# Performance work log

Hardware: AMD Instinct MI355X
Metric: run time of the kernel (lower is better)

The kernel has to match this reference:

```python
import jax, jax.numpy as jnp
import numpy as np

N = 100000      # nodes
E = 1600000     # directed edges
F_IN = 128      # node feature dim
H = 128         # hidden dim
C = 16          # classes


def setup_inputs() -> dict:
    key = jax.random.key(0)
    ks = jax.random.split(key, 8)
    s = 1.0 / np.sqrt(H)
    return {
        "x": jax.random.normal(ks[0], (N, F_IN), dtype=jnp.float32),
        "edge_index": jax.random.randint(ks[1], (2, E), 0, N, dtype=jnp.int32),
        "W1": jax.random.normal(ks[2], (F_IN, H), dtype=jnp.float32) * s,
        "b1": jnp.zeros((H,), jnp.float32),
        "W2": jax.random.normal(ks[3], (H, H), dtype=jnp.float32) * s,
        "b2": jnp.zeros((H,), jnp.float32),
        "W3": jax.random.normal(ks[4], (H, H), dtype=jnp.float32) * s,
        "b3": jnp.zeros((H,), jnp.float32),
        "Wfc": jax.random.normal(ks[5], (H, C), dtype=jnp.float32) * s,
        "bfc": jnp.zeros((C,), jnp.float32),
    }


def _gcn_conv(x, W, b, src, dst, norm):
    # x' = b + scatter_add over edges of norm * (x @ W)[src] into dst
    h = x @ W                                   # [N, H] dense GEMM
    msg = h[src] * norm[:, None]                # [E+N, H] gather + scale
    out = jax.ops.segment_sum(msg, dst, num_segments=N)  # scatter-add
    return out + b


def reference(x, edge_index, W1, b1, W2, b2, W3, b3, Wfc, bfc):
    loops = jnp.arange(N, dtype=edge_index.dtype)
    src = jnp.concatenate([edge_index[0], loops])   # [E+N] with self-loops
    dst = jnp.concatenate([edge_index[1], loops])
    # symmetric normalization deg^{-1/2}[src] * deg^{-1/2}[dst] (PyG default)
    deg = jax.ops.segment_sum(jnp.ones_like(dst, dtype=x.dtype), dst, num_segments=N)
    dinv = jax.lax.rsqrt(deg)                       # deg >= 1 due to self-loops
    norm = dinv[src] * dinv[dst]

    h = jax.nn.elu(_gcn_conv(x, W1, b1, src, dst, norm))   # dropout is identity in eval
    h = jax.nn.elu(_gcn_conv(h, W2, b2, src, dst, norm))
    h = jax.nn.elu(_gcn_conv(h, W3, b3, src, dst, norm))
    logits = h @ Wfc + bfc                                  # [N, C]
    return jax.nn.log_softmax(logits, axis=-1)
```

## Files before the change

kernel.cpp:

```cpp
#include <hip/hip_runtime.h>
#include <math.h>

#define HDIM 128
#define CDIM 16
#define CAP 48
#define ASTR 136
#define HSTR 132
#define NBINS 256
#define TILE 4096
#define NPBMAX 512
#define SORTCAP 7424

typedef unsigned short u16;
typedef unsigned int u32;
typedef __attribute__((ext_vector_type(8))) short short8;
typedef __attribute__((ext_vector_type(4))) float f32x4;
typedef __attribute__((ext_vector_type(2))) float f32x2;

__device__ inline u16 f2bf(float f) {
  u32 u = __float_as_uint(f);
  u += 0x7fffu + ((u >> 16) & 1u);
  return (u16)(u >> 16);
}
__device__ inline float bf_lo(u32 p) { return __uint_as_float(p << 16); }
__device__ inline float bf_hi(u32 p) { return __uint_as_float(p & 0xffff0000u); }
__device__ inline u32 pack2(float a, float b) {
  return (u32)f2bf(a) | ((u32)f2bf(b) << 16);
}
__device__ inline u32 cvtpk(float a, float b) {
  u32 r;
  asm("v_cvt_pk_bf16_f32 %0, %1, %2" : "=v"(r) : "v"(a), "v"(b));
  return r;
}
__device__ inline void acc_word(f32x2& acc, u32 w) {
  f32x2 x;
  x.x = __uint_as_float(w << 16);
  x.y = __uint_as_float(w & 0xffff0000u);
  asm("v_pk_add_f32 %0, %1, %2" : "=v"(acc) : "v"(x), "v"(acc));
}


__global__ __launch_bounds__(256) void bin_kernel(const int* __restrict__ ei,
                                                  int* __restrict__ cursor,
                                                  u32* __restrict__ bins,
                                                  int binCap, int E, int npb, int nbE,
                                                  int nbW, int N,
                                                  const float* __restrict__ W0,
                                                  const float* __restrict__ W1,
                                                  const float* __restrict__ W2,
                                                  u16* __restrict__ Wt,
                                                  u16* __restrict__ Arow,
                                                  u16* __restrict__ Brow) {
  int tid = threadIdx.x;
  if (blockIdx.x >= nbE) {
    if (blockIdx.x >= nbE + nbW) {
      if (tid < 16) ((uint4*)Arow)[tid] = make_uint4(0, 0, 0, 0);
      else if (tid < 32) ((uint4*)Brow)[tid - 16] = make_uint4(0, 0, 0, 0);
      return;
    }
    int t = (blockIdx.x - nbE) * 256 + tid;
    int which = t >> 14, idx = t & 16383;
    int n = idx >> 7, k = idx & 127;
    const float* W = which == 0 ? W0 : (which == 1 ? W1 : W2);
    Wt[(size_t)which * HDIM * HDIM + n * HDIM + k] = f2bf(W[k * HDIM + n]);
    return;
  }
  __shared__ u32 eds32[TILE];
  __shared__ u32 srt[TILE];
  __shared__ unsigned char bid[TILE];
  __shared__ int hist[NBINS], lbase[NBINS + 1], gbase[NBINS], rnk[NBINS];
  int t0 = blockIdx.x * TILE;
  int n = min(TILE, E - t0);
  hist[tid] = 0;
  rnk[tid] = 0;
  __syncthreads();
  for (int i = tid; i < n; i += 256) {
    int s = ei[t0 + i];
    int d = ei[E + t0 + i];
    int b = d / npb;
    eds32[i] = ((u32)(d - b * npb) << 17) | (u32)s;
    bid[i] = (unsigned char)b;
    atomicAdd(&hist[b], 1);
  }
  __syncthreads();
  int h = hist[tid];
  lbase[tid] = h;
  __syncthreads();
#pragma unroll
  for (int off = 1; off < 256; off <<= 1) {
    int v = tid >= off ? lbase[tid - off] : 0;
    __syncthreads();
    lbase[tid] += v;
    __syncthreads();
  }
  int ex = lbase[tid] - h;
  __syncthreads();
  lbase[tid] = ex;
  if (tid == 255) lbase[256] = ex + h;
  gbase[tid] = h ? atomicAdd(&cursor[tid], h) : 0;
  __syncthreads();
  for (int i = tid; i < n; i += 256) {
    int b = bid[i];
    int r = lbase[b] + atomicAdd(&rnk[b], 1);
    srt[r] = eds32[i];
  }
  __syncthreads();
  for (int i = tid; i < n; i += 256) {
    int lo = 0, hi = 255;
#pragma unroll
    for (int k = 0; k < 8; ++k) {
      int mid = (lo + hi + 1) >> 1;
      if (lbase[mid] <= i) lo = mid; else hi = mid - 1;
    }
    int r = gbase[lo] + (i - lbase[lo]);
    if (r < binCap) bins[(size_t)lo * binCap + r] = srt[i];
  }
}

__global__ __launch_bounds__(256) void fill2_kernel(const u32* __restrict__ bins,
                                                    const int* __restrict__ cursor,
                                                    int binCap, int npb,
                                                    int* __restrict__ deg,
                                                    int* __restrict__ csr, int N) {
  __shared__ int hist[NPBMAX];
  __shared__ int base[NPBMAX + 1];
  __shared__ int sorted[SORTCAP];
  int b = blockIdx.x;
  int tid = threadIdx.x;
  int n0 = b * npb;
  int nn = min(npb, N - n0);
  if (nn <= 0) return;
  int cnt = min(min(cursor[b], binCap), SORTCAP);
  const u32* eb = bins + (size_t)b * binCap;
  for (int i = tid; i < nn; i += 256) hist[i] = 0;
  __syncthreads();
  for (int i = tid; i < cnt; i += 256) atomicAdd(&hist[eb[i] >> 17], 1);
  __syncthreads();
  if (tid == 0) {
    int s = 0;
    for (int i = 0; i < nn; ++i) { base[i] = s; s += hist[i]; }
    base[nn] = s;
  }
  __syncthreads();
  for (int i = tid; i < nn; i += 256) hist[i] = 0;
  __syncthreads();
  for (int i = tid; i < cnt; i += 256) {
    u32 w = eb[i];
    int loc = w >> 17;
    sorted[base[loc] + atomicAdd(&hist[loc], 1)] = (int)(w & 0x1FFFFu);
  }
  __syncthreads();
  for (int i = tid; i < nn; i += 256) deg[n0 + i] = base[i + 1] - base[i];
  int total = nn * CAP;
  int* cout = csr + (size_t)n0 * CAP;
  for (int i = tid; i < total; i += 256) {
    int loc = (int)(((u32)(i >> 4) * 21846u) >> 16);
    int j = i - loc * CAP;
    int s0 = base[loc];
    int dc = min(base[loc + 1] - s0, CAP);
    cout[i] = j < dc ? sorted[s0 + j] : N;
  }
}


template <bool FP32IN>
__global__ __launch_bounds__(256) void gemm_k(const void* __restrict__ Xv,
                                              const u16* __restrict__ Wt,
                                              const int* __restrict__ deg,
                                              u16* __restrict__ G, int N) {
  __shared__ u16 As[64 * ASTR];
  __shared__ u16 Wsm[128 * ASTR];
  int tid = threadIdx.x;
  int row0 = blockIdx.x * 64;

  {
    int r = tid >> 2, c = tid & 3;
    int rg = row0 + r;
    if (rg >= N) rg = N - 1;
    uint4* dst = (uint4*)(As + r * ASTR + c * 32);
    if (FP32IN) {
      const float4* src = (const float4*)((const float*)Xv + (size_t)rg * HDIM + c * 32);
#pragma unroll
      for (int j = 0; j < 4; ++j) {
        float4 a = src[2 * j], b = src[2 * j + 1];
        uint4 o;
        o.x = pack2(a.x, a.y); o.y = pack2(a.z, a.w);
        o.z = pack2(b.x, b.y); o.w = pack2(b.z, b.w);
        dst[j] = o;
      }
    } else {
      const uint4* src = (const uint4*)((const u16*)Xv + (size_t)rg * HDIM + c * 32);
      dst[0] = src[0]; dst[1] = src[1]; dst[2] = src[2]; dst[3] = src[3];
    }
  }
  {
    int r = tid >> 1, h = tid & 1;
    const uint4* src = (const uint4*)(Wt + r * HDIM + h * 64);
    uint4* dst = (uint4*)(Wsm + r * ASTR + h * 64);
#pragma unroll
    for (int i = 0; i < 8; ++i) dst[i] = src[i];
  }
  __syncthreads();

  int w = tid >> 6;
  int l = tid & 63;
  int m = l & 15, q = l >> 4;

  f32x4 acc[8];
#pragma unroll
  for (int i = 0; i < 8; ++i) acc[i] = (f32x4){0.f, 0.f, 0.f, 0.f};

#pragma unroll
  for (int kc = 0; kc < 4; ++kc) {
    short8 af = *(const short8*)(As + (w * 16 + m) * ASTR + kc * 32 + q * 8);
#pragma unroll
    for (int nt = 0; nt < 8; ++nt) {
      short8 bfr = *(const short8*)(Wsm + (nt * 16 + m) * ASTR + kc * 32 + q * 8);
      acc[nt] = __builtin_amdgcn_mfma_f32_16x16x32_bf16(af, bfr, acc[nt], 0, 0, 0);
    }
  }
  __syncthreads();

  float dv[4];
#pragma unroll
  for (int r = 0; r < 4; ++r) {
    int rg = row0 + w * 16 + q * 4 + r;
    dv[r] = rsqrtf((float)(deg[rg < N ? rg : N - 1] + 1));
  }
#pragma unroll
  for (int nt = 0; nt < 8; ++nt)
#pragma unroll
    for (int r = 0; r < 4; ++r)
      As[(w * 16 + q * 4 + r) * ASTR + nt * 16 + m] = f2bf(acc[nt][r] * dv[r]);
  __syncthreads();

  {
    int r = tid >> 2, c = tid & 3;
    int rg = row0 + r;
    if (rg < N) {
      uint4* dst = (uint4*)(G + (size_t)rg * HDIM + c * 32);
      const uint4* src = (const uint4*)(As + r * ASTR + c * 32);
      dst[0] = src[0]; dst[1] = src[1]; dst[2] = src[2]; dst[3] = src[3];
    }
  }
}


__device__ inline void gather16(const u16* __restrict__ G, const int* __restrict__ deg,
                                const int* __restrict__ csr,
                                const float4* __restrict__ b4, int node, int l, float* v) {
  const char* Gb = (const char*)G;
  f32x2 p0, p1, p2, p3;
  {
    uint4 sr = *(const uint4*)(Gb + ((size_t)node << 8) + (l << 4));
    p0.x = bf_lo(sr.x); p0.y = bf_hi(sr.x);
    p1.x = bf_lo(sr.y); p1.y = bf_hi(sr.y);
    p2.x = bf_lo(sr.z); p2.y = bf_hi(sr.z);
    p3.x = bf_lo(sr.w); p3.y = bf_hi(sr.w);
  }
  int dfull = deg[node];
  int d = min(dfull, CAP);
  int dp = (d + 7) & ~7;
  const int* row = csr + (size_t)node * CAP;
  int i0 = row[l];
  int i1 = d > 16 ? row[16 + l] : 0;
  int i2 = d > 32 ? row[32 + l] : 0;

#define GLD(u) (*(const uint4*)(Gb + (((u32)(u)) << 8) + (l << 4)))
#define AW(gv) { acc_word(p0, gv.x); acc_word(p1, gv.y); acc_word(p2, gv.z); acc_word(p3, gv.w); }
  for (int k = 0; k < dp; k += 8) {
    int s = k < 16 ? i0 : (k < 32 ? i1 : i2);
    int bl = k & 15;
    int u0 = __shfl(s, bl + 0, 16), u1 = __shfl(s, bl + 1, 16);
    int u2 = __shfl(s, bl + 2, 16), u3 = __shfl(s, bl + 3, 16);
    int u4 = __shfl(s, bl + 4, 16), u5 = __shfl(s, bl + 5, 16);
    int u6 = __shfl(s, bl + 6, 16), u7 = __shfl(s, bl + 7, 16);
    uint4 g0 = GLD(u0), g1 = GLD(u1), g2 = GLD(u2), g3 = GLD(u3);
    uint4 g4 = GLD(u4), g5 = GLD(u5), g6 = GLD(u6), g7 = GLD(u7);
    AW(g0) AW(g1) AW(g2) AW(g3) AW(g4) AW(g5) AW(g6) AW(g7)
  }
#undef AW
#undef GLD
  float dvn = rsqrtf((float)(dfull + 1));
  float4 b0 = b4[l * 2], b1 = b4[l * 2 + 1];
  v[0] = fmaf(dvn, p0.x, b0.x); v[1] = fmaf(dvn, p0.y, b0.y);
  v[2] = fmaf(dvn, p1.x, b0.z); v[3] = fmaf(dvn, p1.y, b0.w);
  v[4] = fmaf(dvn, p2.x, b1.x); v[5] = fmaf(dvn, p2.y, b1.y);
  v[6] = fmaf(dvn, p3.x, b1.z); v[7] = fmaf(dvn, p3.y, b1.w);
#pragma unroll
  for (int j = 0; j < 8; ++j) v[j] = v[j] > 0.f ? v[j] : __expf(v[j]) - 1.f;
}


__global__ __launch_bounds__(256) void agg_gemm(const u16* __restrict__ G,
                                                const int* __restrict__ deg,
                                                const int* __restrict__ csr,
                                                const float* __restrict__ b,
                                                const u16* __restrict__ Wn,
                                                u16* __restrict__ Gout, int N) {
  __shared__ u16 As[16 * ASTR];
  __shared__ float dvs[16];
  int tid = threadIdx.x;
  int node0 = blockIdx.x * 16;
  int lr = tid >> 4, l = tid & 15;
  int node = node0 + lr;
  if (tid < 16) dvs[tid] = rsqrtf((float)(deg[min(node0 + tid, N - 1)] + 1));
  if (node < N) {
    float v[8];
    gather16(G, deg, csr, (const float4*)b, node, l, v);
    uint4 o;
    o.x = cvtpk(v[0], v[1]); o.y = cvtpk(v[2], v[3]);
    o.z = cvtpk(v[4], v[5]); o.w = cvtpk(v[6], v[7]);
    *(uint4*)(As + lr * ASTR + l * 8) = o;
  } else {
    uint4 z = make_uint4(0, 0, 0, 0);
    *(uint4*)(As + lr * ASTR + l * 8) = z;
  }
  __syncthreads();

  int w = tid >> 6;
  int lw = tid & 63;
  int m = lw & 15, q = lw >> 4;
  f32x4 acc0 = (f32x4){0.f, 0.f, 0.f, 0.f};
  f32x4 acc1 = (f32x4){0.f, 0.f, 0.f, 0.f};
#pragma unroll
  for (int kc = 0; kc < 4; ++kc) {
    short8 af = *(const short8*)(As + m * ASTR + kc * 32 + q * 8);
    short8 b0 = *(const short8*)(Wn + ((w * 2 + 0) * 16 + m) * HDIM + kc * 32 + q * 8);
    short8 b1 = *(const short8*)(Wn + ((w * 2 + 1) * 16 + m) * HDIM + kc * 32 + q * 8);
    acc0 = __builtin_amdgcn_mfma_f32_16x16x32_bf16(af, b0, acc0, 0, 0, 0);
    acc1 = __builtin_amdgcn_mfma_f32_16x16x32_bf16(af, b1, acc1, 0, 0, 0);
  }
  __syncthreads();

#pragma unroll
  for (int r = 0; r < 4; ++r) {
    float dvr = dvs[q * 4 + r];
    As[(q * 4 + r) * ASTR + (w * 2 + 0) * 16 + m] = f2bf(acc0[r] * dvr);
    As[(q * 4 + r) * ASTR + (w * 2 + 1) * 16 + m] = f2bf(acc1[r] * dvr);
  }
  __syncthreads();

  {
    int r = tid >> 4, c = tid & 15;
    if (node0 + r < N)
      *(uint4*)(Gout + (size_t)(node0 + r) * HDIM + c * 8) =
          *(const uint4*)(As + r * ASTR + c * 8);
  }
}


__global__ __launch_bounds__(256) void agg_fc(const u16* __restrict__ G,
                                              const int* __restrict__ deg,
                                              const int* __restrict__ csr,
                                              const float* __restrict__ b,
                                              const float* __restrict__ Wfc,
                                              const float* __restrict__ bfc,
                                              float* __restrict__ out, int N) {
  __shared__ float Hs[16 * HSTR];
  __shared__ float Wl[HDIM * CDIM];
  int tid = threadIdx.x;
  for (int i = tid; i < HDIM * CDIM; i += 256) Wl[i] = Wfc[i];

  int node0 = blockIdx.x * 16;
  int lr = tid >> 4, l = tid & 15;
  int node = node0 + lr;
  if (node < N) {
    float v[8];
    gather16(G, deg, csr, (const float4*)b, node, l, v);
    float4* dst = (float4*)(Hs + lr * HSTR + l * 8);
    dst[0] = make_float4(v[0], v[1], v[2], v[3]);
    dst[1] = make_float4(v[4], v[5], v[6], v[7]);
  }
  __syncthreads();

  int rg = node0 + lr;
  if (rg >= N) return;
  int c = l;
  const float* hrow = Hs + lr * HSTR;
  float acc = bfc[c];
#pragma unroll 4
  for (int k4 = 0; k4 < 32; ++k4) {
    float4 g = *(const float4*)(hrow + k4 * 4);
    const float* wk = Wl + (k4 * 4) * CDIM + c;
    acc = fmaf(g.x, wk[0 * CDIM], acc);
    acc = fmaf(g.y, wk[1 * CDIM], acc);
    acc = fmaf(g.z, wk[2 * CDIM], acc);
    acc = fmaf(g.w, wk[3 * CDIM], acc);
  }
  float mx = acc;
  for (int off = 8; off >= 1; off >>= 1) mx = fmaxf(mx, __shfl_xor(mx, off, 16));
  float ex = __expf(acc - mx);
  float ssum = ex;
  for (int off = 8; off >= 1; off >>= 1) ssum += __shfl_xor(ssum, off, 16);
  out[(size_t)rg * CDIM + c] = (acc - mx) - __logf(ssum);
}


extern "C" void kernel_launch(void* const* d_in, const int* in_sizes, int n_in,
                              void* d_out, int out_size, void* d_ws, size_t ws_size,
                              hipStream_t stream) {
  const float* x   = (const float*)d_in[0];
  const int*   ei  = (const int*)d_in[1];
  const float* W1  = (const float*)d_in[2];
  const float* b1  = (const float*)d_in[3];
  const float* W2  = (const float*)d_in[4];
  const float* b2  = (const float*)d_in[5];
  const float* W3  = (const float*)d_in[6];
  const float* b3  = (const float*)d_in[7];
  const float* Wfc = (const float*)d_in[8];
  const float* bfc = (const float*)d_in[9];

  const int N = in_sizes[0] / HDIM;
  const int E = in_sizes[1] / 2;
  const int npb = (N + NBINS - 1) / NBINS;
  const int binCap = (E + NBINS - 1) / NBINS + 1024;
  const int nbE = (E + TILE - 1) / TILE;
  const int nbW = 3 * HDIM * HDIM / 256;

  char* ws = (char*)d_ws;
  size_t off = 0;
  auto alloc = [&](size_t bytes) -> void* {
    void* p = ws + off;
    off += (bytes + 511) & ~(size_t)511;
    return p;
  };
  int*   deg    = (int*)alloc((size_t)N * 4);
  int*   cursor = (int*)alloc((size_t)NBINS * 4);
  int*   csr    = (int*)alloc((size_t)N * CAP * 4);
  u32*   bins   = (u32*)alloc((size_t)NBINS * binCap * 4);
  u16*   Wt     = (u16*)alloc((size_t)3 * HDIM * HDIM * 2);
  u16*   A      = (u16*)alloc((size_t)(N + 1) * HDIM * 2);
  u16*   B      = (u16*)alloc((size_t)(N + 1) * HDIM * 2);

  hipMemsetAsync(cursor, 0, (size_t)NBINS * 4, stream);
  bin_kernel<<<nbE + nbW + 1, 256, 0, stream>>>(ei, cursor, bins, binCap, E, npb, nbE, nbW,
                                                N, W1, W2, W3, Wt,
                                                A + (size_t)N * HDIM, B + (size_t)N * HDIM);
  fill2_kernel<<<NBINS, 256, 0, stream>>>(bins, cursor, binCap, npb, deg, csr, N);

  int grid64 = (N + 63) / 64;
  int grid16 = (N + 15) / 16;
  gemm_k<true><<<grid64, 256, 0, stream>>>(x, Wt, deg, A, N);
  agg_gemm<<<grid16, 256, 0, stream>>>(A, deg, csr, b1, Wt + HDIM * HDIM, B, N);
  agg_gemm<<<grid16, 256, 0, stream>>>(B, deg, csr, b2, Wt + 2 * HDIM * HDIM, A, N);
  agg_fc<<<grid16, 256, 0, stream>>>(A, deg, csr, b3, Wfc, bfc, (float*)d_out, N);
}
```

Baseline: 369.8 us.

## Reorder GCN layers as aggregate-then-transform and drop standalone first GEMM

Uses associativity (A·X)·W = A·(X·W) so each layer aggregates first and then applies the weight GEMM, with bias and ELU moved into the post-GEMM epilogue. The separate first-layer gemm_k kernel is removed; instead x is prescaled by deg^-1/2 and converted to bf16 inside the fill kernel's extra blocks. The last aggregation kernel now also does the W3 MFMA before the FC head. Degree is computed with global atomics in the binning kernel so the prescale can run alongside CSR construction. The cost is per-edge global atomics on deg and an extra bf16 copy of x.

After: 417.2 us. +12.8%, slower.

```diff
diff --git a/kernel.cpp b/kernel.cpp
--- a/kernel.cpp
+++ b/kernel.cpp
@@ -24,9 +24,6 @@
 }
 __device__ inline float bf_lo(u32 p) { return __uint_as_float(p << 16); }
 __device__ inline float bf_hi(u32 p) { return __uint_as_float(p & 0xffff0000u); }
-__device__ inline u32 pack2(float a, float b) {
-  return (u32)f2bf(a) | ((u32)f2bf(b) << 16);
-}
 __device__ inline u32 cvtpk(float a, float b) {
   u32 r;
   asm("v_cvt_pk_bf16_f32 %0, %1, %2" : "=v"(r) : "v"(a), "v"(b));
@@ -44,18 +41,20 @@
                                                   int* __restrict__ cursor,
                                                   u32* __restrict__ bins,
                                                   int binCap, int E, int npb, int nbE,
-                                                  int nbW, int N,
+                                                  int nbW, int N, int* __restrict__ deg,
                                                   const float* __restrict__ W0,
                                                   const float* __restrict__ W1,
                                                   const float* __restrict__ W2,
                                                   u16* __restrict__ Wt,
                                                   u16* __restrict__ Arow,
-                                                  u16* __restrict__ Brow) {
+                                                  u16* __restrict__ Brow,
+                                                  u16* __restrict__ Xrow) {
   int tid = threadIdx.x;
   if (blockIdx.x >= nbE) {
     if (blockIdx.x >= nbE + nbW) {
       if (tid < 16) ((uint4*)Arow)[tid] = make_uint4(0, 0, 0, 0);
       else if (tid < 32) ((uint4*)Brow)[tid - 16] = make_uint4(0, 0, 0, 0);
+      else if (tid < 48) ((uint4*)Xrow)[tid - 32] = make_uint4(0, 0, 0, 0);
       return;
     }
     int t = (blockIdx.x - nbE) * 256 + tid;
@@ -81,6 +80,7 @@
     eds32[i] = ((u32)(d - b * npb) << 17) | (u32)s;
     bid[i] = (unsigned char)b;
     atomicAdd(&hist[b], 1);
+    atomicAdd(&deg[d], 1);
   }
   __syncthreads();
   int h = hist[tid];
@@ -120,13 +120,32 @@
 __global__ __launch_bounds__(256) void fill2_kernel(const u32* __restrict__ bins,
                                                     const int* __restrict__ cursor,
                                                     int binCap, int npb,
-                                                    int* __restrict__ deg,
-                                                    int* __restrict__ csr, int N) {
+                                                    const int* __restrict__ deg,
+                                                    int* __restrict__ csr, int N,
+                                                    const float* __restrict__ x,
+                                                    u16* __restrict__ Xc) {
+  int tid = threadIdx.x;
+  if (blockIdx.x >= NBINS) {
+    int rg = (blockIdx.x - NBINS) * 64 + (tid >> 2);
+    if (rg >= N) return;
+    int c = tid & 3;
+    float dv = rsqrtf((float)(deg[rg] + 1));
+    const float4* src = (const float4*)(x + (size_t)rg * HDIM + c * 32);
+    uint4* dst = (uint4*)(Xc + (size_t)rg * HDIM + c * 32);
+#pragma unroll
+    for (int j = 0; j < 4; ++j) {
+      float4 a = src[2 * j], b = src[2 * j + 1];
+      uint4 o;
+      o.x = cvtpk(dv * a.x, dv * a.y); o.y = cvtpk(dv * a.z, dv * a.w);
+      o.z = cvtpk(dv * b.x, dv * b.y); o.w = cvtpk(dv * b.z, dv * b.w);
+      dst[j] = o;
+    }
+    return;
+  }
   __shared__ int hist[NPBMAX];
   __shared__ int base[NPBMAX + 1];
   __shared__ int sorted[SORTCAP];
   int b = blockIdx.x;
-  int tid = threadIdx.x;
   int n0 = b * npb;
   int nn = min(npb, N - n0);
   if (nn <= 0) return;
@@ -150,7 +169,6 @@
     sorted[base[loc] + atomicAdd(&hist[loc], 1)] = (int)(w & 0x1FFFFu);
   }
   __syncthreads();
-  for (int i = tid; i < nn; i += 256) deg[n0 + i] = base[i + 1] - base[i];
   int total = nn * CAP;
   int* cout = csr + (size_t)n0 * CAP;
   for (int i = tid; i < total; i += 256) {
@@ -163,92 +181,8 @@
 }
 
 
-template <bool FP32IN>
-__global__ __launch_bounds__(256) void gemm_k(const void* __restrict__ Xv,
-                                              const u16* __restrict__ Wt,
-                                              const int* __restrict__ deg,
-                                              u16* __restrict__ G, int N) {
-  __shared__ u16 As[64 * ASTR];
-  __shared__ u16 Wsm[128 * ASTR];
-  int tid = threadIdx.x;
-  int row0 = blockIdx.x * 64;
-
-  {
-    int r = tid >> 2, c = tid & 3;
-    int rg = row0 + r;
-    if (rg >= N) rg = N - 1;
-    uint4* dst = (uint4*)(As + r * ASTR + c * 32);
-    if (FP32IN) {
-      const float4* src = (const float4*)((const float*)Xv + (size_t)rg * HDIM + c * 32);
-#pragma unroll
-      for (int j = 0; j < 4; ++j) {
-        float4 a = src[2 * j], b = src[2 * j + 1];
-        uint4 o;
-        o.x = pack2(a.x, a.y); o.y = pack2(a.z, a.w);
-        o.z = pack2(b.x, b.y); o.w = pack2(b.z, b.w);
-        dst[j] = o;
-      }
-    } else {
-      const uint4* src = (const uint4*)((const u16*)Xv + (size_t)rg * HDIM + c * 32);
-      dst[0] = src[0]; dst[1] = src[1]; dst[2] = src[2]; dst[3] = src[3];
-    }
-  }
-  {
-    int r = tid >> 1, h = tid & 1;
-    const uint4* src = (const uint4*)(Wt + r * HDIM + h * 64);
-    uint4* dst = (uint4*)(Wsm + r * ASTR + h * 64);
-#pragma unroll
-    for (int i = 0; i < 8; ++i) dst[i] = src[i];
-  }
-  __syncthreads();
-
-  int w = tid >> 6;
-  int l = tid & 63;
-  int m = l & 15, q = l >> 4;
-
-  f32x4 acc[8];
-#pragma unroll
-  for (int i = 0; i < 8; ++i) acc[i] = (f32x4){0.f, 0.f, 0.f, 0.f};
-
-#pragma unroll
-  for (int kc = 0; kc < 4; ++kc) {
-    short8 af = *(const short8*)(As + (w * 16 + m) * ASTR + kc * 32 + q * 8);
-#pragma unroll
-    for (int nt = 0; nt < 8; ++nt) {
-      short8 bfr = *(const short8*)(Wsm + (nt * 16 + m) * ASTR + kc * 32 + q * 8);
-      acc[nt] = __builtin_amdgcn_mfma_f32_16x16x32_bf16(af, bfr, acc[nt], 0, 0, 0);
-    }
-  }
-  __syncthreads();
-
-  float dv[4];
-#pragma unroll
-  for (int r = 0; r < 4; ++r) {
-    int rg = row0 + w * 16 + q * 4 + r;
-    dv[r] = rsqrtf((float)(deg[rg < N ? rg : N - 1] + 1));
-  }
-#pragma unroll
-  for (int nt = 0; nt < 8; ++nt)
-#pragma unroll
-    for (int r = 0; r < 4; ++r)
-      As[(w * 16 + q * 4 + r) * ASTR + nt * 16 + m] = f2bf(acc[nt][r] * dv[r]);
-  __syncthreads();
-
-  {
-    int r = tid >> 2, c = tid & 3;
-    int rg = row0 + r;
-    if (rg < N) {
-      uint4* dst = (uint4*)(G + (size_t)rg * HDIM + c * 32);
-      const uint4* src = (const uint4*)(As + r * ASTR + c * 32);
-      dst[0] = src[0]; dst[1] = src[1]; dst[2] = src[2]; dst[3] = src[3];
-    }
-  }
-}
-
-
 __device__ inline void gather16(const u16* __restrict__ G, const int* __restrict__ deg,
-                                const int* __restrict__ csr,
-                                const float4* __restrict__ b4, int node, int l, float* v) {
+                                const int* __restrict__ csr, int node, int l, float* v) {
   const char* Gb = (const char*)G;
   f32x2 p0, p1, p2, p3;
   {
@@ -282,13 +216,10 @@
 #undef AW
 #undef GLD
   float dvn = rsqrtf((float)(dfull + 1));
-  float4 b0 = b4[l * 2], b1 = b4[l * 2 + 1];
-  v[0] = fmaf(dvn, p0.x, b0.x); v[1] = fmaf(dvn, p0.y, b0.y);
-  v[2] = fmaf(dvn, p1.x, b0.z); v[3] = fmaf(dvn, p1.y, b0.w);
-  v[4] = fmaf(dvn, p2.x, b1.x); v[5] = fmaf(dvn, p2.y, b1.y);
-  v[6] = fmaf(dvn, p3.x, b1.z); v[7] = fmaf(dvn, p3.y, b1.w);
-#pragma unroll
-  for (int j = 0; j < 8; ++j) v[j] = v[j] > 0.f ? v[j] : __expf(v[j]) - 1.f;
+  v[0] = dvn * p0.x; v[1] = dvn * p0.y;
+  v[2] = dvn * p1.x; v[3] = dvn * p1.y;
+  v[4] = dvn * p2.x; v[5] = dvn * p2.y;
+  v[6] = dvn * p3.x; v[7] = dvn * p3.y;
 }
 
 
@@ -307,14 +238,13 @@
   if (tid < 16) dvs[tid] = rsqrtf((float)(deg[min(node0 + tid, N - 1)] + 1));
   if (node < N) {
     float v[8];
-    gather16(G, deg, csr, (const float4*)b, node, l, v);
+    gather16(G, deg, csr, node, l, v);
     uint4 o;
     o.x = cvtpk(v[0], v[1]); o.y = cvtpk(v[2], v[3]);
     o.z = cvtpk(v[4], v[5]); o.w = cvtpk(v[6], v[7]);
     *(uint4*)(As + lr * ASTR + l * 8) = o;
   } else {
-    uint4 z = make_uint4(0, 0, 0, 0);
-    *(uint4*)(As + lr * ASTR + l * 8) = z;
+    *(uint4*)(As + lr * ASTR + l * 8) = make_uint4(0, 0, 0, 0);
   }
   __syncthreads();
 
@@ -333,11 +263,14 @@
   }
   __syncthreads();
 
+  float bc0 = b[(w * 2 + 0) * 16 + m], bc1 = b[(w * 2 + 1) * 16 + m];
 #pragma unroll
   for (int r = 0; r < 4; ++r) {
     float dvr = dvs[q * 4 + r];
-    As[(q * 4 + r) * ASTR + (w * 2 + 0) * 16 + m] = f2bf(acc0[r] * dvr);
-    As[(q * 4 + r) * ASTR + (w * 2 + 1) * 16 + m] = f2bf(acc1[r] * dvr);
+    float h0 = acc0[r] + bc0; h0 = h0 > 0.f ? h0 : __expf(h0) - 1.f;
+    float h1 = acc1[r] + bc1; h1 = h1 > 0.f ? h1 : __expf(h1) - 1.f;
+    As[(q * 4 + r) * ASTR + (w * 2 + 0) * 16 + m] = f2bf(h0 * dvr);
+    As[(q * 4 + r) * ASTR + (w * 2 + 1) * 16 + m] = f2bf(h1 * dvr);
   }
   __syncthreads();
 
@@ -353,10 +286,12 @@
 __global__ __launch_bounds__(256) void agg_fc(const u16* __restrict__ G,
                                               const int* __restrict__ deg,
                                               const int* __restrict__ csr,
-                                              const float* __restrict__ b,
+                                              const float* __restrict__ b3,
+                                              const u16* __restrict__ W3t,
                                               const float* __restrict__ Wfc,
                                               const float* __restrict__ bfc,
                                               float* __restrict__ out, int N) {
+  __shared__ u16 As[16 * ASTR];
   __shared__ float Hs[16 * HSTR];
   __shared__ float Wl[HDIM * CDIM];
   int tid = threadIdx.x;
@@ -367,10 +302,36 @@
   int node = node0 + lr;
   if (node < N) {
     float v[8];
-    gather16(G, deg, csr, (const float4*)b, node, l, v);
-    float4* dst = (float4*)(Hs + lr * HSTR + l * 8);
-    dst[0] = make_float4(v[0], v[1], v[2], v[3]);
-    dst[1] = make_float4(v[4], v[5], v[6], v[7]);
+    gather16(G, deg, csr, node, l, v);
+    uint4 o;
+    o.x = cvtpk(v[0], v[1]); o.y = cvtpk(v[2], v[3]);
+    o.z = cvtpk(v[4], v[5]); o.w = cvtpk(v[6], v[7]);
+    *(uint4*)(As + lr * ASTR + l * 8) = o;
+  } else {
+    *(uint4*)(As + lr * ASTR + l * 8) = make_uint4(0, 0, 0, 0);
+  }
+  __syncthreads();
+
+  int w = tid >> 6;
+  int lw = tid & 63;
+  int m = lw & 15, q = lw >> 4;
+  f32x4 acc0 = (f32x4){0.f, 0.f, 0.f, 0.f};
+  f32x4 acc1 = (f32x4){0.f, 0.f, 0.f, 0.f};
+#pragma unroll
+  for (int kc = 0; kc < 4; ++kc) {
+    short8 af = *(const short8*)(As + m * ASTR + kc * 32 + q * 8);
+    short8 w0 = *(const short8*)(W3t + ((w * 2 + 0) * 16 + m) * HDIM + kc * 32 + q * 8);
+    short8 w1 = *(const short8*)(W3t + ((w * 2 + 1) * 16 + m) * HDIM + kc * 32 + q * 8);
+    acc0 = __builtin_amdgcn_mfma_f32_16x16x32_bf16(af, w0, acc0, 0, 0, 0);
+    acc1 = __builtin_amdgcn_mfma_f32_16x16x32_bf16(af, w1, acc1, 0, 0, 0);
+  }
+  float bc0 = b3[(w * 2 + 0) * 16 + m], bc1 = b3[(w * 2 + 1) * 16 + m];
+#pragma unroll
+  for (int r = 0; r < 4; ++r) {
+    float h0 = acc0[r] + bc0; h0 = h0 > 0.f ? h0 : __expf(h0) - 1.f;
+    float h1 = acc1[r] + bc1; h1 = h1 > 0.f ? h1 : __expf(h1) - 1.f;
+    Hs[(q * 4 + r) * HSTR + (w * 2 + 0) * 16 + m] = h0;
+    Hs[(q * 4 + r) * HSTR + (w * 2 + 1) * 16 + m] = h1;
   }
   __syncthreads();
 
@@ -417,6 +378,7 @@
   const int binCap = (E + NBINS - 1) / NBINS + 1024;
   const int nbE = (E + TILE - 1) / TILE;
   const int nbW = 3 * HDIM * HDIM / 256;
+  const int nbC = (N + 63) / 64;
 
   char* ws = (char*)d_ws;
   size_t off = 0;
@@ -430,19 +392,21 @@
   int*   csr    = (int*)alloc((size_t)N * CAP * 4);
   u32*   bins   = (u32*)alloc((size_t)NBINS * binCap * 4);
   u16*   Wt     = (u16*)alloc((size_t)3 * HDIM * HDIM * 2);
+  u16*   Xc     = (u16*)alloc((size_t)(N + 1) * HDIM * 2);
   u16*   A      = (u16*)alloc((size_t)(N + 1) * HDIM * 2);
   u16*   B      = (u16*)alloc((size_t)(N + 1) * HDIM * 2);
 
-  hipMemsetAsync(cursor, 0, (size_t)NBINS * 4, stream);
+  size_t degPad = (((size_t)N * 4) + 511) & ~(size_t)511;
+  hipMemsetAsync(deg, 0, degPad + 1024, stream);
   bin_kernel<<<nbE + nbW + 1, 256, 0, stream>>>(ei, cursor, bins, binCap, E, npb, nbE, nbW,
-                                                N, W1, W2, W3, Wt,
-                                                A + (size_t)N * HDIM, B + (size_t)N * HDIM);
-  fill2_kernel<<<NBINS, 256, 0, stream>>>(bins, cursor, binCap, npb, deg, csr, N);
-
-  int grid64 = (N + 63) / 64;
+                                                N, deg, W1, W2, W3, Wt,
+                                                A + (size_t)N * HDIM, B + (size_t)N * HDIM,
+                                                Xc + (size_t)N * HDIM);
+  fill2_kernel<<<NBINS + nbC, 256, 0, stream>>>(bins, cursor, binCap, npb, deg, csr, N, x, Xc);
+
   int grid16 = (N + 15) / 16;
-  gemm_k<true><<<grid64, 256, 0, stream>>>(x, Wt, deg, A, N);
-  agg_gemm<<<grid16, 256, 0, stream>>>(A, deg, csr, b1, Wt + HDIM * HDIM, B, N);
-  agg_gemm<<<grid16, 256, 0, stream>>>(B, deg, csr, b2, Wt + 2 * HDIM * HDIM, A, N);
-  agg_fc<<<grid16, 256, 0, stream>>>(A, deg, csr, b3, Wfc, bfc, (float*)d_out, N);
-}
+  agg_gemm<<<grid16, 256, 0, stream>>>(Xc, deg, csr, b1, Wt, A, N);
+  agg_gemm<<<grid16, 256, 0, stream>>>(A, deg, csr, b2, Wt + HDIM * HDIM, B, N);
+  agg_fc<<<grid16, 256, 0, stream>>>(B, deg, csr, b3, Wt + 2 * HDIM * HDIM, Wfc, bfc,
+                                     (float*)d_out, N);
+}
```
